# Kernel optimization log

Measured on AMD Instinct MI355X. Metric: run time of the kernel, lower is better.

## Reference

```python
import jax, jax.numpy as jnp
import numpy as np

N = 8_388_608
C = 3  # 3 sentiment classes; |argmax - y| == 2 <=> class-0/class-2 confusion


def setup_inputs() -> dict:
    key = jax.random.key(0)
    k1, k2 = jax.random.split(key)
    logits = jax.random.normal(k1, (N, C), dtype=jnp.float32)
    # original module expects log-softmax outputs
    pre = jax.nn.log_softmax(logits, axis=-1)
    y_true = jax.random.randint(k2, (N,), 0, C, dtype=jnp.int64)
    weight = jnp.float32(2.0)
    return {"pre": pre, "y_true": y_true, "weight": weight}


def reference(pre, y_true, weight):
    # gather log-prob of true class: pre[i, y_true[i]]
    picked = jnp.take_along_axis(pre, y_true[:, None], axis=1)[:, 0]  # [N]
    pred = jnp.argmax(pre, axis=-1)                                   # [N]
    # penalize opposite-polarity mistakes (|pred - y| == 2)
    penal = jnp.abs(pred - y_true) == 2                               # [N] bool
    w = jnp.where(penal, weight, jnp.float32(1.0))                    # [N]
    return -jnp.sum(w * picked) / jnp.float32(pre.shape[0])
```

## Files before the change

### kernel.cpp

```cpp
#include <hip/hip_runtime.h>


typedef float v4f __attribute__((ext_vector_type(4)));

#define N_ROWS   8388608
#define BLOCK    256
#define GRID     1024
#define WPB      (BLOCK / 64)
#define NWAVES   (GRID * WPB)
#define CHUNK    256
#define NITER    (N_ROWS / (NWAVES * CHUNK))
#define ROWS_PW  (CHUNK * NITER)

__global__ __launch_bounds__(BLOCK) void nll_main(
        const float* __restrict__ pre,
        const int*   __restrict__ y_true,
        const float* __restrict__ wptr,
        float*       __restrict__ partial) {
    __shared__ float tile[WPB][2][768];
    __shared__ float red[WPB];

    const float wgt  = wptr[0];
    const int   t    = threadIdx.x;
    const int   lane = t & 63;
    const int   wv   = t >> 6;
    const int   W    = (int)blockIdx.x * WPB + wv;

    const v4f* __restrict__ pre4 = (const v4f*)pre;
    const int fbW = W * (ROWS_PW * 3 / 4);
    const int ybW = W * ROWS_PW;

    v4f v[3][3];
    int yv[3][4];

    #pragma unroll
    for (int p = 0; p < 2; ++p) {
        const int fb = fbW + p * 192;
        const int yb = ybW + p * 256;
        v[p][0] = __builtin_nontemporal_load(pre4 + fb +       lane);
        v[p][1] = __builtin_nontemporal_load(pre4 + fb +  64 + lane);
        v[p][2] = __builtin_nontemporal_load(pre4 + fb + 128 + lane);
        yv[p][0] = __builtin_nontemporal_load(y_true + yb +       lane);
        yv[p][1] = __builtin_nontemporal_load(y_true + yb +  64 + lane);
        yv[p][2] = __builtin_nontemporal_load(y_true + yb + 128 + lane);
        yv[p][3] = __builtin_nontemporal_load(y_true + yb + 192 + lane);
    }

    float acc = 0.0f;
    #pragma unroll
    for (int k = 0; k < NITER; ++k) {
        const int b  = k % 3;
        const int nb = (k + 2) % 3;

        if (k + 2 < NITER) {
            const int fb = fbW + (k + 2) * 192;
            const int yb = ybW + (k + 2) * 256;
            v[nb][0] = __builtin_nontemporal_load(pre4 + fb +       lane);
            v[nb][1] = __builtin_nontemporal_load(pre4 + fb +  64 + lane);
            v[nb][2] = __builtin_nontemporal_load(pre4 + fb + 128 + lane);
            yv[nb][0] = __builtin_nontemporal_load(y_true + yb +       lane);
            yv[nb][1] = __builtin_nontemporal_load(y_true + yb +  64 + lane);
            yv[nb][2] = __builtin_nontemporal_load(y_true + yb + 128 + lane);
            yv[nb][3] = __builtin_nontemporal_load(y_true + yb + 192 + lane);
        }

        float* slice = tile[wv][k & 1];
        v4f*   s4    = (v4f*)slice;
        s4[       lane] = v[b][0];
        s4[ 64 +  lane] = v[b][1];
        s4[128 +  lane] = v[b][2];

        asm volatile("s_waitcnt lgkmcnt(0)" ::: "memory");

        #pragma unroll
        for (int m = 0; m < 4; ++m) {
            const int   w0 = 3 * lane + 192 * m;
            const float p0 = slice[w0 + 0];
            const float p1 = slice[w0 + 1];
            const float p2 = slice[w0 + 2];
            const int   tt = yv[b][m];
            const float picked = (tt == 0) ? p0 : ((tt == 1) ? p1 : p2);
            int   prd = 0;
            float mx  = p0;
            if (p1 > mx) { mx = p1; prd = 1; }
            if (p2 > mx) { prd = 2; }
            const bool penal = (prd - tt == 2) || (tt - prd == 2);
            acc += (penal ? wgt : 1.0f) * picked;
        }
    }

    #pragma unroll
    for (int off = 32; off > 0; off >>= 1)
        acc += __shfl_down(acc, off, 64);

    if (lane == 0) red[wv] = acc;
    __syncthreads();

    if (t == 0)
        partial[blockIdx.x] = red[0] + red[1] + red[2] + red[3];
}

__global__ __launch_bounds__(256) void nll_reduce(
        const float* __restrict__ partial,
        float*       __restrict__ out) {
    const float4 p = ((const float4*)partial)[threadIdx.x];
    float s = p.x + p.y + p.z + p.w;
    #pragma unroll
    for (int off = 32; off > 0; off >>= 1)
        s += __shfl_down(s, off, 64);

    __shared__ float r[4];
    if ((threadIdx.x & 63) == 0) r[threadIdx.x >> 6] = s;
    __syncthreads();
    if (threadIdx.x == 0)
        out[0] = (r[0] + r[1] + r[2] + r[3]) * (-1.0f / (float)N_ROWS);
}

extern "C" void kernel_launch(void* const* d_in, const int* in_sizes, int n_in,
                              void* d_out, int out_size, void* d_ws, size_t ws_size,
                              hipStream_t stream) {
    const float* pre  = (const float*)d_in[0];
    const int*   y    = (const int*)d_in[1];
    const float* wptr = (const float*)d_in[2];
    float* ws  = (float*)d_ws;
    float* out = (float*)d_out;

    nll_main<<<GRID, BLOCK, 0, stream>>>(pre, y, wptr, ws);
    nll_reduce<<<1, 256, 0, stream>>>(ws, out);
}
```

Before: 159.5 us.

## Load rows per-lane as contiguous float4 triples, drop LDS transpose, double grid

New measurement: 171.5 us. 1.08x slower.

```diff
diff --git a/kernel.cpp b/kernel.cpp
--- a/kernel.cpp
+++ b/kernel.cpp
@@ -2,24 +2,31 @@
 
 
 typedef float v4f __attribute__((ext_vector_type(4)));
+typedef int   v4i __attribute__((ext_vector_type(4)));
 
 #define N_ROWS   8388608
 #define BLOCK    256
-#define GRID     1024
+#define GRID     2048
 #define WPB      (BLOCK / 64)
 #define NWAVES   (GRID * WPB)
-#define CHUNK    256
-#define NITER    (N_ROWS / (NWAVES * CHUNK))
-#define ROWS_PW  (CHUNK * NITER)
+#define ROWS_PW  (N_ROWS / NWAVES)
+#define NITER    4
+
+__device__ __forceinline__ float row3(float p0, float p1, float p2, int tt, float wgt) {
+    const float picked = (tt == 0) ? p0 : ((tt == 1) ? p1 : p2);
+    int   prd = 0;
+    float mx  = p0;
+    if (p1 > mx) { mx = p1; prd = 1; }
+    if (p2 > mx) { prd = 2; }
+    const bool penal = (prd - tt == 2) || (tt - prd == 2);
+    return (penal ? wgt : 1.0f) * picked;
+}
 
 __global__ __launch_bounds__(BLOCK) void nll_main(
         const float* __restrict__ pre,
         const int*   __restrict__ y_true,
         const float* __restrict__ wptr,
         float*       __restrict__ partial) {
-    __shared__ float tile[WPB][2][768];
-    __shared__ float red[WPB];
-
     const float wgt  = wptr[0];
     const int   t    = threadIdx.x;
     const int   lane = t & 63;
@@ -27,23 +34,20 @@
     const int   W    = (int)blockIdx.x * WPB + wv;
 
     const v4f* __restrict__ pre4 = (const v4f*)pre;
-    const int fbW = W * (ROWS_PW * 3 / 4);
-    const int ybW = W * ROWS_PW;
+    const v4i* __restrict__ y4   = (const v4i*)y_true;
+
+    const int fbW = W * 768 + 3 * lane;
+    const int ybW = W * 256 + lane;
 
     v4f v[3][3];
-    int yv[3][4];
+    v4i y[3];
 
     #pragma unroll
     for (int p = 0; p < 2; ++p) {
-        const int fb = fbW + p * 192;
-        const int yb = ybW + p * 256;
-        v[p][0] = __builtin_nontemporal_load(pre4 + fb +       lane);
-        v[p][1] = __builtin_nontemporal_load(pre4 + fb +  64 + lane);
-        v[p][2] = __builtin_nontemporal_load(pre4 + fb + 128 + lane);
-        yv[p][0] = __builtin_nontemporal_load(y_true + yb +       lane);
-        yv[p][1] = __builtin_nontemporal_load(y_true + yb +  64 + lane);
-        yv[p][2] = __builtin_nontemporal_load(y_true + yb + 128 + lane);
-        yv[p][3] = __builtin_nontemporal_load(y_true + yb + 192 + lane);
+        v[p][0] = pre4[fbW + p * 192 + 0];
+        v[p][1] = pre4[fbW + p * 192 + 1];
+        v[p][2] = pre4[fbW + p * 192 + 2];
+        y[p]    = y4[ybW + p * 64];
     }
 
     float acc = 0.0f;
@@ -53,46 +57,25 @@
         const int nb = (k + 2) % 3;
 
         if (k + 2 < NITER) {
-            const int fb = fbW + (k + 2) * 192;
-            const int yb = ybW + (k + 2) * 256;
-            v[nb][0] = __builtin_nontemporal_load(pre4 + fb +       lane);
-            v[nb][1] = __builtin_nontemporal_load(pre4 + fb +  64 + lane);
-            v[nb][2] = __builtin_nontemporal_load(pre4 + fb + 128 + lane);
-            yv[nb][0] = __builtin_nontemporal_load(y_true + yb +       lane);
-            yv[nb][1] = __builtin_nontemporal_load(y_true + yb +  64 + lane);
-            yv[nb][2] = __builtin_nontemporal_load(y_true + yb + 128 + lane);
-            yv[nb][3] = __builtin_nontemporal_load(y_true + yb + 192 + lane);
+            v[nb][0] = pre4[fbW + (k + 2) * 192 + 0];
+            v[nb][1] = pre4[fbW + (k + 2) * 192 + 1];
+            v[nb][2] = pre4[fbW + (k + 2) * 192 + 2];
+            y[nb]    = y4[ybW + (k + 2) * 64];
         }
 
-        float* slice = tile[wv][k & 1];
-        v4f*   s4    = (v4f*)slice;
-        s4[       lane] = v[b][0];
-        s4[ 64 +  lane] = v[b][1];
-        s4[128 +  lane] = v[b][2];
-
-        asm volatile("s_waitcnt lgkmcnt(0)" ::: "memory");
-
-        #pragma unroll
-        for (int m = 0; m < 4; ++m) {
-            const int   w0 = 3 * lane + 192 * m;
-            const float p0 = slice[w0 + 0];
-            const float p1 = slice[w0 + 1];
-            const float p2 = slice[w0 + 2];
-            const int   tt = yv[b][m];
-            const float picked = (tt == 0) ? p0 : ((tt == 1) ? p1 : p2);
-            int   prd = 0;
-            float mx  = p0;
-            if (p1 > mx) { mx = p1; prd = 1; }
-            if (p2 > mx) { prd = 2; }
-            const bool penal = (prd - tt == 2) || (tt - prd == 2);
-            acc += (penal ? wgt : 1.0f) * picked;
-        }
+        const v4f a  = v[b][0], c = v[b][1], d = v[b][2];
+        const v4i yy = y[b];
+        acc += row3(a.x, a.y, a.z, yy.x, wgt);
+        acc += row3(a.w, c.x, c.y, yy.y, wgt);
+        acc += row3(c.z, c.w, d.x, yy.z, wgt);
+        acc += row3(d.y, d.z, d.w, yy.w, wgt);
     }
 
     #pragma unroll
     for (int off = 32; off > 0; off >>= 1)
         acc += __shfl_down(acc, off, 64);
 
+    __shared__ float red[WPB];
     if (lane == 0) red[wv] = acc;
     __syncthreads();
 
@@ -100,7 +83,7 @@
         partial[blockIdx.x] = red[0] + red[1] + red[2] + red[3];
 }
 
-__global__ __launch_bounds__(256) void nll_reduce(
+__global__ __launch_bounds__(512) void nll_reduce(
         const float* __restrict__ partial,
         float*       __restrict__ out) {
     const float4 p = ((const float4*)partial)[threadIdx.x];
@@ -109,11 +92,15 @@
     for (int off = 32; off > 0; off >>= 1)
         s += __shfl_down(s, off, 64);
 
-    __shared__ float r[4];
+    __shared__ float r[8];
     if ((threadIdx.x & 63) == 0) r[threadIdx.x >> 6] = s;
     __syncthreads();
-    if (threadIdx.x == 0)
-        out[0] = (r[0] + r[1] + r[2] + r[3]) * (-1.0f / (float)N_ROWS);
+    if (threadIdx.x == 0) {
+        float tot = 0.0f;
+        #pragma unroll
+        for (int i = 0; i < 8; ++i) tot += r[i];
+        out[0] = tot * (-1.0f / (float)N_ROWS);
+    }
 }
 
 extern "C" void kernel_launch(void* const* d_in, const int* in_sizes, int n_in,
@@ -126,5 +113,5 @@
     float* out = (float*)d_out;
 
     nll_main<<<GRID, BLOCK, 0, stream>>>(pre, y, wptr, ws);
-    nll_reduce<<<1, 256, 0, stream>>>(ws, out);
+    nll_reduce<<<1, 512, 0, stream>>>(ws, out);
 }
```

## Software-pipeline LDS staging one iteration ahead and drop nontemporal loads

Applied to the files above, without the earlier changes.

Result: slower. 176.9 us (+10.9%).

```diff
diff --git a/kernel.cpp b/kernel.cpp
--- a/kernel.cpp
+++ b/kernel.cpp
@@ -30,55 +30,67 @@
     const int fbW = W * (ROWS_PW * 3 / 4);
     const int ybW = W * ROWS_PW;
 
-    v4f v[3][3];
+    v4f v[2][3];
     int yv[3][4];
 
     #pragma unroll
     for (int p = 0; p < 2; ++p) {
         const int fb = fbW + p * 192;
         const int yb = ybW + p * 256;
-        v[p][0] = __builtin_nontemporal_load(pre4 + fb +       lane);
-        v[p][1] = __builtin_nontemporal_load(pre4 + fb +  64 + lane);
-        v[p][2] = __builtin_nontemporal_load(pre4 + fb + 128 + lane);
-        yv[p][0] = __builtin_nontemporal_load(y_true + yb +       lane);
-        yv[p][1] = __builtin_nontemporal_load(y_true + yb +  64 + lane);
-        yv[p][2] = __builtin_nontemporal_load(y_true + yb + 128 + lane);
-        yv[p][3] = __builtin_nontemporal_load(y_true + yb + 192 + lane);
+        v[p][0] = pre4[fb +       lane];
+        v[p][1] = pre4[fb +  64 + lane];
+        v[p][2] = pre4[fb + 128 + lane];
+        yv[p][0] = y_true[yb +       lane];
+        yv[p][1] = y_true[yb +  64 + lane];
+        yv[p][2] = y_true[yb + 128 + lane];
+        yv[p][3] = y_true[yb + 192 + lane];
     }
+    {
+        v4f* s4 = (v4f*)tile[wv][0];
+        s4[       lane] = v[0][0];
+        s4[ 64 +  lane] = v[0][1];
+        s4[128 +  lane] = v[0][2];
+    }
+    asm volatile("s_waitcnt lgkmcnt(0)" ::: "memory");
 
     float acc = 0.0f;
     #pragma unroll
     for (int k = 0; k < NITER; ++k) {
-        const int b  = k % 3;
-        const int nb = (k + 2) % 3;
+        const float* slice = tile[wv][k & 1];
+        float p[4][3];
+        #pragma unroll
+        for (int m = 0; m < 4; ++m) {
+            const int w0 = 3 * lane + 192 * m;
+            p[m][0] = slice[w0 + 0];
+            p[m][1] = slice[w0 + 1];
+            p[m][2] = slice[w0 + 2];
+        }
 
         if (k + 2 < NITER) {
             const int fb = fbW + (k + 2) * 192;
             const int yb = ybW + (k + 2) * 256;
-            v[nb][0] = __builtin_nontemporal_load(pre4 + fb +       lane);
-            v[nb][1] = __builtin_nontemporal_load(pre4 + fb +  64 + lane);
-            v[nb][2] = __builtin_nontemporal_load(pre4 + fb + 128 + lane);
-            yv[nb][0] = __builtin_nontemporal_load(y_true + yb +       lane);
-            yv[nb][1] = __builtin_nontemporal_load(y_true + yb +  64 + lane);
-            yv[nb][2] = __builtin_nontemporal_load(y_true + yb + 128 + lane);
-            yv[nb][3] = __builtin_nontemporal_load(y_true + yb + 192 + lane);
+            v[k & 1][0] = pre4[fb +       lane];
+            v[k & 1][1] = pre4[fb +  64 + lane];
+            v[k & 1][2] = pre4[fb + 128 + lane];
+            yv[(k + 2) % 3][0] = y_true[yb +       lane];
+            yv[(k + 2) % 3][1] = y_true[yb +  64 + lane];
+            yv[(k + 2) % 3][2] = y_true[yb + 128 + lane];
+            yv[(k + 2) % 3][3] = y_true[yb + 192 + lane];
         }
 
-        float* slice = tile[wv][k & 1];
-        v4f*   s4    = (v4f*)slice;
-        s4[       lane] = v[b][0];
-        s4[ 64 +  lane] = v[b][1];
-        s4[128 +  lane] = v[b][2];
+        if (k + 1 < NITER) {
+            v4f* s4 = (v4f*)tile[wv][(k + 1) & 1];
+            s4[       lane] = v[(k + 1) & 1][0];
+            s4[ 64 +  lane] = v[(k + 1) & 1][1];
+            s4[128 +  lane] = v[(k + 1) & 1][2];
+        }
 
         asm volatile("s_waitcnt lgkmcnt(0)" ::: "memory");
 
         #pragma unroll
         for (int m = 0; m < 4; ++m) {
-            const int   w0 = 3 * lane + 192 * m;
-            const float p0 = slice[w0 + 0];
-            const float p1 = slice[w0 + 1];
-            const float p2 = slice[w0 + 2];
-            const int   tt = yv[b][m];
+            const float p0 = p[m][0], p1 = p[m][1], p2 = p[m][2];
+            const int   tt = yv[k % 3][m];
             const float picked = (tt == 0) ? p0 : ((tt == 1) ? p1 : p2);
             int   prd = 0;
             float mx  = p0;
```

## Load logits directly into LDS with global_load_lds triple buffering

Applied to the files above, without the earlier changes.

Result: slower. 175.5 us (+10.0%).

```diff
diff --git a/kernel.cpp b/kernel.cpp
--- a/kernel.cpp
+++ b/kernel.cpp
@@ -2,6 +2,10 @@
 
 
 typedef float v4f __attribute__((ext_vector_type(4)));
+
+#define GLL(gp, lp) __builtin_amdgcn_global_load_lds(                      \
+    (const __attribute__((address_space(1))) void*)(gp),                   \
+    (__attribute__((address_space(3))) void*)(lp), 16, 0, 0)
 
 #define N_ROWS   8388608
 #define BLOCK    256
@@ -17,7 +21,7 @@
         const int*   __restrict__ y_true,
         const float* __restrict__ wptr,
         float*       __restrict__ partial) {
-    __shared__ float tile[WPB][2][768];
+    __shared__ float tile[WPB][3][768];
     __shared__ float red[WPB];
 
     const float wgt  = wptr[0];
@@ -30,47 +34,40 @@
     const int fbW = W * (ROWS_PW * 3 / 4);
     const int ybW = W * ROWS_PW;
 
-    v4f v[3][3];
     int yv[3][4];
 
     #pragma unroll
     for (int p = 0; p < 2; ++p) {
         const int fb = fbW + p * 192;
         const int yb = ybW + p * 256;
-        v[p][0] = __builtin_nontemporal_load(pre4 + fb +       lane);
-        v[p][1] = __builtin_nontemporal_load(pre4 + fb +  64 + lane);
-        v[p][2] = __builtin_nontemporal_load(pre4 + fb + 128 + lane);
-        yv[p][0] = __builtin_nontemporal_load(y_true + yb +       lane);
-        yv[p][1] = __builtin_nontemporal_load(y_true + yb +  64 + lane);
-        yv[p][2] = __builtin_nontemporal_load(y_true + yb + 128 + lane);
-        yv[p][3] = __builtin_nontemporal_load(y_true + yb + 192 + lane);
+        GLL(pre4 + fb +       lane, &tile[wv][p][  0]);
+        GLL(pre4 + fb +  64 + lane, &tile[wv][p][256]);
+        GLL(pre4 + fb + 128 + lane, &tile[wv][p][512]);
+        yv[p][0] = y_true[yb +       lane];
+        yv[p][1] = y_true[yb +  64 + lane];
+        yv[p][2] = y_true[yb + 128 + lane];
+        yv[p][3] = y_true[yb + 192 + lane];
     }
 
     float acc = 0.0f;
     #pragma unroll
     for (int k = 0; k < NITER; ++k) {
-        const int b  = k % 3;
-        const int nb = (k + 2) % 3;
+        if (k < NITER - 1) asm volatile("s_waitcnt vmcnt(7)" ::: "memory");
+        else               asm volatile("s_waitcnt vmcnt(0)" ::: "memory");
+
+        const float* slice = tile[wv][k % 3];
 
         if (k + 2 < NITER) {
             const int fb = fbW + (k + 2) * 192;
             const int yb = ybW + (k + 2) * 256;
-            v[nb][0] = __builtin_nontemporal_load(pre4 + fb +       lane);
-            v[nb][1] = __builtin_nontemporal_load(pre4 + fb +  64 + lane);
-            v[nb][2] = __builtin_nontemporal_load(pre4 + fb + 128 + lane);
-            yv[nb][0] = __builtin_nontemporal_load(y_true + yb +       lane);
-            yv[nb][1] = __builtin_nontemporal_load(y_true + yb +  64 + lane);
-            yv[nb][2] = __builtin_nontemporal_load(y_true + yb + 128 + lane);
-            yv[nb][3] = __builtin_nontemporal_load(y_true + yb + 192 + lane);
+            GLL(pre4 + fb +       lane, &tile[wv][(k + 2) % 3][  0]);
+            GLL(pre4 + fb +  64 + lane, &tile[wv][(k + 2) % 3][256]);
+            GLL(pre4 + fb + 128 + lane, &tile[wv][(k + 2) % 3][512]);
+            yv[(k + 2) % 3][0] = y_true[yb +       lane];
+            yv[(k + 2) % 3][1] = y_true[yb +  64 + lane];
+            yv[(k + 2) % 3][2] = y_true[yb + 128 + lane];
+            yv[(k + 2) % 3][3] = y_true[yb + 192 + lane];
         }
-
-        float* slice = tile[wv][k & 1];
-        v4f*   s4    = (v4f*)slice;
-        s4[       lane] = v[b][0];
-        s4[ 64 +  lane] = v[b][1];
-        s4[128 +  lane] = v[b][2];
-
-        asm volatile("s_waitcnt lgkmcnt(0)" ::: "memory");
 
         #pragma unroll
         for (int m = 0; m < 4; ++m) {
@@ -78,7 +75,7 @@
             const float p0 = slice[w0 + 0];
             const float p1 = slice[w0 + 1];
             const float p2 = slice[w0 + 2];
-            const int   tt = yv[b][m];
+            const int   tt = yv[k % 3][m];
             const float picked = (tt == 0) ? p0 : ((tt == 1) ? p1 : p2);
             int   prd = 0;
             float mx  = p0;
```
